# Kernel optimization log

Hardware: AMD Instinct MI355X
Metric: run time of the kernel (lower is better)

## Reference

```python
import jax, jax.numpy as jnp
import numpy as np

B, C, H, W = 16, 1, 128, 8192
N_MAX = 128
CHIRP_W, PERIOD = 48, 64
W_OUT = N_MAX * CHIRP_W + (N_MAX - 1)  # 6271 compacted columns (chirps + separators)
SEP_CLASS_ID = 2


def setup_inputs() -> dict:
    key = jax.random.key(0)
    k1, k2, k3, k4 = jax.random.split(key, 4)
    x = jax.random.normal(k1, (B, C, H, W), dtype=jnp.float32)
    starts = jnp.arange(N_MAX, dtype=jnp.int32) * PERIOD
    xi = jnp.stack([starts, starts + CHIRP_W], axis=-1)           # (N_MAX, 2)
    xi = jnp.broadcast_to(xi[None], (B, N_MAX, 2)).astype(jnp.int32)
    N = jax.random.randint(k2, (B,), 96, N_MAX + 1, dtype=jnp.int32)
    N = N.at[0].set(N_MAX)  # pin so static W_OUT equals torch's dynamic int(w_max.max())
    xl = jax.random.randint(k3, (B, W), 0, 2, dtype=jnp.int32)
    sep_param = jax.random.normal(k4, (1, 1, 1), dtype=jnp.float32)
    return {"x": x, "xi": xi, "N": N, "xl": xl, "sep_param": sep_param, "w_out": W_OUT}


def _compactify(x, xi, N, xl, sep_param, w_out):
    """Vectorized TinyBird.compactify_data: remove silence, keep chirp blocks,
    insert one separator column between consecutive valid chirps."""
    Bx, Cx, Hx, Wx = x.shape
    n_max = xi.shape[1]
    idx = jnp.arange(n_max, dtype=jnp.int32)[None, :]             # (1, N_max)
    Nb = N.reshape(-1, 1).astype(jnp.int32)
    valid = idx < Nb                                              # (B, N_max)

    s0, e0 = xi[..., 0], xi[..., 1]
    w = jnp.clip(e0 - s0, 0, None)
    w_valid = jnp.where(valid, w, 0)
    csum = jnp.cumsum(w_valid, axis=1)
    sn = csum - w_valid + idx                                     # new start (seps before = idx)
    en = csum + idx                                               # new end
    xi_new = jnp.where(valid[..., None], jnp.stack([sn, en], -1), 0).astype(xi.dtype)

    BIG = jnp.int32(1 << 30)
    en_srt = jnp.where(valid, en, BIG)                            # strictly increasing over valid part
    t = jnp.arange(w_out, dtype=jnp.int32)[None, :]               # (1, w_out)
    # i = number of chirp ends <= t  ->  chirp whose [sn_i, en_i) may contain t
    i = (en_srt[:, :, None] <= t[:, None, :]).sum(axis=1).astype(jnp.int32)  # (B, w_out)
    ic = jnp.clip(i, 0, n_max - 1)
    take = lambda a: jnp.take_along_axis(a, ic, axis=1)
    sn_i, en_i = take(sn), take(en)
    s0_i, e0_i = take(s0), take(e0)
    in_chirp = (i < Nb) & (t >= sn_i) & (en_i > sn_i) & (e0_i > s0_i)
    src = jnp.clip(s0_i + (t - sn_i), 0, Wx - 1)                  # (B, w_out)

    # separator column: t == en_{i-1}, previous chirp is not the last valid one, en < W
    jp = jnp.clip(i - 1, 0, n_max - 1)
    en_prev = jnp.take_along_axis(en, jp, axis=1)
    is_sep = (i >= 1) & (t == en_prev) & ((i - 1) < (Nb - 1)) & (en_prev < Wx)

    x_g = jnp.take_along_axis(x, src[:, None, None, :], axis=3)   # (B, C, H, w_out)
    sep = sep_param[0, 0, 0]
    x_new = jnp.where(in_chirp[:, None, None, :], x_g,
                      jnp.where(is_sep[:, None, None, :], sep, jnp.float32(0)))
    xl_g = jnp.take_along_axis(xl, src, axis=1)
    xl_new = jnp.where(in_chirp, xl_g,
                       jnp.where(is_sep, jnp.asarray(SEP_CLASS_ID, xl.dtype),
                                 jnp.asarray(0, xl.dtype)))
    return x_new, xi_new, xl_new


def reference(x, xi, N, xl, sep_param, w_out):
    return _compactify(x, xi, N, xl, sep_param, w_out)
```

## Files before the change

kernel.cpp:

```cpp
#include <hip/hip_runtime.h>

#define BB     16
#define HH     128
#define WW     8192
#define N_MAXC 128
#define W_OUTC 6271
#define SEP_CLASS 2.0f

#define X_ELEMS (BB * HH * W_OUTC)
#define XI_OFF  (X_ELEMS)
#define XL_OFF  (X_ELEMS + BB * N_MAXC * 2)

#define MAP_BYTES ((size_t)(BB * W_OUTC) * sizeof(int))

#define TCOLS  1024
#define HROWS  16
#define MTILE  896

__global__ __launch_bounds__(256) void tb_meta(const int* __restrict__ xi,
                                               const int* __restrict__ Nv,
                                               const int* __restrict__ xl,
                                               float* __restrict__ out,
                                               int* __restrict__ map) {
    __shared__ int s_s0[N_MAXC], s_e0[N_MAXC], s_scan[N_MAXC], s_sn[N_MAXC], s_en[N_MAXC];
    const int b   = blockIdx.x;
    const int tid = threadIdx.x;
    const int Nb  = Nv[b];

    int wv = 0;
    if (tid < N_MAXC) {
        int2 se = ((const int2*)xi)[b * N_MAXC + tid];
        s_s0[tid] = se.x; s_e0[tid] = se.y;
        int w = se.y - se.x; if (w < 0) w = 0;
        wv = (tid < Nb) ? w : 0;
        s_scan[tid] = wv;
    }
    __syncthreads();
    #pragma unroll
    for (int off = 1; off < N_MAXC; off <<= 1) {
        int v = 0;
        if (tid < N_MAXC && tid >= off) v = s_scan[tid - off];
        __syncthreads();
        if (tid < N_MAXC) s_scan[tid] += v;
        __syncthreads();
    }
    if (tid < N_MAXC) {
        int c = s_scan[tid];
        s_sn[tid] = c - wv + tid;
        s_en[tid] = c + tid;
    }
    __syncthreads();

    if (blockIdx.y == 0 && tid < N_MAXC) {
        const bool valid = tid < Nb;
        out[XI_OFF + (b * N_MAXC + tid) * 2 + 0] = valid ? (float)s_sn[tid] : 0.0f;
        out[XI_OFF + (b * N_MAXC + tid) * 2 + 1] = valid ? (float)s_en[tid] : 0.0f;
    }

    const int t_lo = blockIdx.y * MTILE;
    const int t_hi = (t_lo + MTILE < W_OUTC) ? t_lo + MTILE : W_OUTC;
    for (int t = t_lo + tid; t < t_hi; t += 256) {
        int lo = 0, hi = Nb;
        while (lo < hi) { int mid = (lo + hi) >> 1; if (s_en[mid] <= t) lo = mid + 1; else hi = mid; }
        const int i  = lo;
        const int ic = (i < N_MAXC - 1) ? i : (N_MAXC - 1);
        int m = -2;
        if (i < Nb) {
            int sn = s_sn[ic], en = s_en[ic];
            if (t >= sn && en > sn && s_e0[ic] > s_s0[ic]) {
                int src = s_s0[ic] + (t - sn);
                src = src < 0 ? 0 : (src > WW - 1 ? WW - 1 : src);
                m = src;
            }
        }
        if (m == -2 && i >= 1) {
            int ep = s_en[i - 1];
            if (t == ep && (i - 1) < (Nb - 1) && ep < WW) m = -1;
        }
        if (map) map[b * W_OUTC + t] = m;
        float v = (m >= 0) ? (float)xl[b * WW + m] : ((m == -1) ? SEP_CLASS : 0.0f);
        out[XL_OFF + b * W_OUTC + t] = v;
    }
}

__global__ __launch_bounds__(256) void tb_gather(const float* __restrict__ x,
                                                 const int* __restrict__ map,
                                                 const float* __restrict__ sep_param,
                                                 float* __restrict__ out) {
    __shared__ int s_map[TCOLS];
    const int t0   = blockIdx.x * TCOLS;
    const int h0   = blockIdx.y * HROWS;
    const int b    = blockIdx.z;
    const int tid  = threadIdx.x;
    const int tmax = W_OUTC - t0;
    const float sep = sep_param[0];

    for (int j = tid; j < TCOLS; j += 256) {
        int t = t0 + j;
        s_map[j] = (t < W_OUTC) ? map[b * W_OUTC + t] : -2;
    }
    __syncthreads();

    const float* xb = x   + (size_t)(b * HH + h0) * WW;
    float*       ob = out + (size_t)(b * HH + h0) * W_OUTC + t0;

    if (tmax >= TCOLS) {
        #pragma unroll 4
        for (int r = 0; r < HROWS; ++r) {
            const float* xr   = xb + (size_t)r * WW;
            float*       orow = ob + (size_t)r * W_OUTC;
            #pragma unroll
            for (int k = 0; k < 4; ++k) {
                const int j = k * 256 + tid;
                const int m = s_map[j];
                const int a = (m >= 0) ? m : 0;
                const float xv = xr[a];
                orow[j] = (m >= 0) ? xv : ((m == -1) ? sep : 0.0f);
            }
        }
    } else {
        #pragma unroll 4
        for (int r = 0; r < HROWS; ++r) {
            const float* xr   = xb + (size_t)r * WW;
            float*       orow = ob + (size_t)r * W_OUTC;
            #pragma unroll
            for (int k = 0; k < 4; ++k) {
                const int j = k * 256 + tid;
                if (j < tmax) {
                    const int m = s_map[j];
                    const int a = (m >= 0) ? m : 0;
                    const float xv = xr[a];
                    orow[j] = (m >= 0) ? xv : ((m == -1) ? sep : 0.0f);
                }
            }
        }
    }
}

#define FTILE   512
#define FHCHUNK 32

__device__ __forceinline__ void fb_scan(const int* __restrict__ xi, int b, int Nb,
                                        int* s_s0, int* s_e0, int* s_sn, int* s_en, int tid) {
    if (tid < N_MAXC) {
        s_s0[tid] = xi[(b * N_MAXC + tid) * 2 + 0];
        s_e0[tid] = xi[(b * N_MAXC + tid) * 2 + 1];
    }
    __syncthreads();
    if (tid == 0) {
        int c = 0;
        for (int i = 0; i < N_MAXC; ++i) {
            int w = s_e0[i] - s_s0[i]; if (w < 0) w = 0;
            int wvv = (i < Nb) ? w : 0;
            c += wvv;
            s_sn[i] = c - wvv + i;
            s_en[i] = c + i;
        }
    }
    __syncthreads();
}

__global__ __launch_bounds__(256) void tb_gather_tiled(const float* __restrict__ x,
                                                       const int* __restrict__ xi,
                                                       const int* __restrict__ Nv,
                                                       const float* __restrict__ sep_param,
                                                       float* __restrict__ out) {
    __shared__ int s_s0[N_MAXC], s_e0[N_MAXC], s_sn[N_MAXC], s_en[N_MAXC];
    __shared__ int s_map[FTILE];
    const int b = blockIdx.z, h0 = blockIdx.y * FHCHUNK, t0 = blockIdx.x * FTILE;
    const int tid = threadIdx.x, Nb = Nv[b];
    fb_scan(xi, b, Nb, s_s0, s_e0, s_sn, s_en, tid);
    for (int j = tid; j < FTILE; j += 256) {
        int t = t0 + j, m = -2;
        if (t < W_OUTC) {
            int lo = 0, hi = Nb;
            while (lo < hi) { int mid = (lo + hi) >> 1; if (s_en[mid] <= t) lo = mid + 1; else hi = mid; }
            int i = lo, ic = (i < N_MAXC - 1) ? i : (N_MAXC - 1);
            if (i < Nb) {
                int sn = s_sn[ic], en = s_en[ic];
                if (t >= sn && en > sn && s_e0[ic] > s_s0[ic]) {
                    int src = s_s0[ic] + (t - sn);
                    m = src < 0 ? 0 : (src > WW - 1 ? WW - 1 : src);
                }
            }
            if (m == -2 && i >= 1) {
                int ep = s_en[i - 1];
                if (t == ep && (i - 1) < (Nb - 1) && ep < WW) m = -1;
            }
        }
        s_map[j] = m;
    }
    __syncthreads();
    const float sep = sep_param[0];
    const float* xb = x + (size_t)b * HH * WW;
    float* ob = out + (size_t)b * HH * W_OUTC;
    for (int r = 0; r < FHCHUNK; ++r) {
        const int h = h0 + r;
        const float* xr = xb + (size_t)h * WW;
        float* orow = ob + (size_t)h * W_OUTC;
        for (int j = tid; j < FTILE; j += 256) {
            int t = t0 + j;
            if (t < W_OUTC) {
                int m = s_map[j];
                orow[t] = (m >= 0) ? xr[m] : ((m == -1) ? sep : 0.0f);
            }
        }
    }
}

extern "C" void kernel_launch(void* const* d_in, const int* in_sizes, int n_in,
                              void* d_out, int out_size, void* d_ws, size_t ws_size,
                              hipStream_t stream) {
    const float* x   = (const float*)d_in[0];
    const int*   xi  = (const int*)  d_in[1];
    const int*   Nv  = (const int*)  d_in[2];
    const int*   xl  = (const int*)  d_in[3];
    const float* sep = (const float*)d_in[4];
    float*       out = (float*)d_out;

    const bool use_ws = (ws_size >= MAP_BYTES) && (d_ws != nullptr);
    int* map = use_ws ? (int*)d_ws : nullptr;

    tb_meta<<<dim3(BB, 7), dim3(256), 0, stream>>>(xi, Nv, xl, out, map);

    if (use_ws) {
        dim3 grid((W_OUTC + TCOLS - 1) / TCOLS, HH / HROWS, BB);
        tb_gather<<<grid, dim3(256), 0, stream>>>(x, map, sep, out);
    } else {
        dim3 grid((W_OUTC + FTILE - 1) / FTILE, HH / FHCHUNK, BB);
        tb_gather_tiled<<<grid, dim3(256), 0, stream>>>(x, xi, Nv, sep, out);
    }
}
```

Before: 153.0 us.

## Flatten gather into float4 output stores with batched loads per thread

Replaces the 2D-tiled gather that staged the column map in shared memory with a flat grid-stride kernel. Each thread handles eight 4-element output chunks, loading all map entries and gathered x values up front before issuing float4 stores, which raises memory-level parallelism and widens the writes. The meta kernel's tile is shrunk so it launches more blocks. In exchange, map reads now go to global memory (cached) rather than shared, per-element index math includes integer division, and the row-wrap handling is needed because W_OUT is odd, so a float4 chunk can span two rows.

```diff
diff --git a/kernel.cpp b/kernel.cpp
--- a/kernel.cpp
+++ b/kernel.cpp
@@ -10,12 +10,15 @@
 #define X_ELEMS (BB * HH * W_OUTC)
 #define XI_OFF  (X_ELEMS)
 #define XL_OFF  (X_ELEMS + BB * N_MAXC * 2)
+#define NCHUNKS (X_ELEMS / 4)
 
 #define MAP_BYTES ((size_t)(BB * W_OUTC) * sizeof(int))
 
-#define TCOLS  1024
-#define HROWS  16
-#define MTILE  896
+#define GBLK  1568
+#define GSTR  (GBLK * 256)
+#define GITER 8
+
+#define MTILE 512
 
 __global__ __launch_bounds__(256) void tb_meta(const int* __restrict__ xi,
                                                const int* __restrict__ Nv,
@@ -83,82 +86,64 @@
     }
 }
 
-__global__ __launch_bounds__(256) void tb_gather(const float* __restrict__ x,
-                                                 const int* __restrict__ map,
-                                                 const float* __restrict__ sep_param,
-                                                 float* __restrict__ out) {
-    __shared__ int s_map[TCOLS];
-    const int t0   = blockIdx.x * TCOLS;
-    const int h0   = blockIdx.y * HROWS;
-    const int b    = blockIdx.z;
-    const int tid  = threadIdx.x;
-    const int tmax = W_OUTC - t0;
+__global__ __launch_bounds__(256) void tb_gather_flat(const float* __restrict__ x,
+                                                      const int* __restrict__ map,
+                                                      const float* __restrict__ sep_param,
+                                                      float* __restrict__ out) {
+    const unsigned gtid = blockIdx.x * 256u + threadIdx.x;
     const float sep = sep_param[0];
 
-    for (int j = tid; j < TCOLS; j += 256) {
-        int t = t0 + j;
-        s_map[j] = (t < W_OUTC) ? map[b * W_OUTC + t] : -2;
-    }
-    __syncthreads();
-
-    const float* xb = x   + (size_t)(b * HH + h0) * WW;
-    float*       ob = out + (size_t)(b * HH + h0) * W_OUTC + t0;
-
-    if (tmax >= TCOLS) {
-        #pragma unroll 4
-        for (int r = 0; r < HROWS; ++r) {
-            const float* xr   = xb + (size_t)r * WW;
-            float*       orow = ob + (size_t)r * W_OUTC;
-            #pragma unroll
-            for (int k = 0; k < 4; ++k) {
-                const int j = k * 256 + tid;
-                const int m = s_map[j];
-                const int a = (m >= 0) ? m : 0;
-                const float xv = xr[a];
-                orow[j] = (m >= 0) ? xv : ((m == -1) ? sep : 0.0f);
-            }
-        }
-    } else {
-        #pragma unroll 4
-        for (int r = 0; r < HROWS; ++r) {
-            const float* xr   = xb + (size_t)r * WW;
-            float*       orow = ob + (size_t)r * W_OUTC;
-            #pragma unroll
-            for (int k = 0; k < 4; ++k) {
-                const int j = k * 256 + tid;
-                if (j < tmax) {
-                    const int m = s_map[j];
-                    const int a = (m >= 0) ? m : 0;
-                    const float xv = xr[a];
-                    orow[j] = (m >= 0) ? xv : ((m == -1) ? sep : 0.0f);
-                }
-            }
+    unsigned rowA[GITER], colA[GITER];
+    int      mv[GITER][4];
+    float    xv[GITER][4];
+
+    #pragma unroll
+    for (int j = 0; j < GITER; ++j) {
+        unsigned c = gtid + (unsigned)j * (unsigned)GSTR;
+        if (c >= (unsigned)NCHUNKS) c = NCHUNKS - 1;
+        const unsigned flat = c * 4u;
+        const unsigned bh   = flat / (unsigned)W_OUTC;
+        rowA[j] = bh;
+        colA[j] = flat - bh * (unsigned)W_OUTC;
+    }
+    #pragma unroll
+    for (int j = 0; j < GITER; ++j) {
+        #pragma unroll
+        for (int k = 0; k < 4; ++k) {
+            unsigned tk = colA[j] + (unsigned)k;
+            unsigned r  = rowA[j];
+            if (tk >= (unsigned)W_OUTC) { tk -= (unsigned)W_OUTC; r += 1u; }
+            mv[j][k] = map[(r >> 7) * (unsigned)W_OUTC + tk];
+        }
+    }
+    #pragma unroll
+    for (int j = 0; j < GITER; ++j) {
+        #pragma unroll
+        for (int k = 0; k < 4; ++k) {
+            unsigned tk = colA[j] + (unsigned)k;
+            unsigned r  = rowA[j];
+            if (tk >= (unsigned)W_OUTC) r += 1u;
+            const int m = mv[j][k];
+            const unsigned a = (m >= 0) ? (unsigned)m : 0u;
+            xv[j][k] = x[((size_t)r << 13) + a];
+        }
+    }
+    #pragma unroll
+    for (int j = 0; j < GITER; ++j) {
+        const unsigned c = gtid + (unsigned)j * (unsigned)GSTR;
+        if (c < (unsigned)NCHUNKS) {
+            float4 v;
+            v.x = (mv[j][0] >= 0) ? xv[j][0] : ((mv[j][0] == -1) ? sep : 0.0f);
+            v.y = (mv[j][1] >= 0) ? xv[j][1] : ((mv[j][1] == -1) ? sep : 0.0f);
+            v.z = (mv[j][2] >= 0) ? xv[j][2] : ((mv[j][2] == -1) ? sep : 0.0f);
+            v.w = (mv[j][3] >= 0) ? xv[j][3] : ((mv[j][3] == -1) ? sep : 0.0f);
+            ((float4*)out)[c] = v;
         }
     }
 }
 
 #define FTILE   512
 #define FHCHUNK 32
-
-__device__ __forceinline__ void fb_scan(const int* __restrict__ xi, int b, int Nb,
-                                        int* s_s0, int* s_e0, int* s_sn, int* s_en, int tid) {
-    if (tid < N_MAXC) {
-        s_s0[tid] = xi[(b * N_MAXC + tid) * 2 + 0];
-        s_e0[tid] = xi[(b * N_MAXC + tid) * 2 + 1];
-    }
-    __syncthreads();
-    if (tid == 0) {
-        int c = 0;
-        for (int i = 0; i < N_MAXC; ++i) {
-            int w = s_e0[i] - s_s0[i]; if (w < 0) w = 0;
-            int wvv = (i < Nb) ? w : 0;
-            c += wvv;
-            s_sn[i] = c - wvv + i;
-            s_en[i] = c + i;
-        }
-    }
-    __syncthreads();
-}
 
 __global__ __launch_bounds__(256) void tb_gather_tiled(const float* __restrict__ x,
                                                        const int* __restrict__ xi,
@@ -169,7 +154,22 @@
     __shared__ int s_map[FTILE];
     const int b = blockIdx.z, h0 = blockIdx.y * FHCHUNK, t0 = blockIdx.x * FTILE;
     const int tid = threadIdx.x, Nb = Nv[b];
-    fb_scan(xi, b, Nb, s_s0, s_e0, s_sn, s_en, tid);
+    if (tid < N_MAXC) {
+        s_s0[tid] = xi[(b * N_MAXC + tid) * 2 + 0];
+        s_e0[tid] = xi[(b * N_MAXC + tid) * 2 + 1];
+    }
+    __syncthreads();
+    if (tid == 0) {
+        int c = 0;
+        for (int i = 0; i < N_MAXC; ++i) {
+            int w = s_e0[i] - s_s0[i]; if (w < 0) w = 0;
+            int wvv = (i < Nb) ? w : 0;
+            c += wvv;
+            s_sn[i] = c - wvv + i;
+            s_en[i] = c + i;
+        }
+    }
+    __syncthreads();
     for (int j = tid; j < FTILE; j += 256) {
         int t = t0 + j, m = -2;
         if (t < W_OUTC) {
@@ -221,11 +221,10 @@
     const bool use_ws = (ws_size >= MAP_BYTES) && (d_ws != nullptr);
     int* map = use_ws ? (int*)d_ws : nullptr;
 
-    tb_meta<<<dim3(BB, 7), dim3(256), 0, stream>>>(xi, Nv, xl, out, map);
+    tb_meta<<<dim3(BB, 13), dim3(256), 0, stream>>>(xi, Nv, xl, out, map);
 
     if (use_ws) {
-        dim3 grid((W_OUTC + TCOLS - 1) / TCOLS, HH / HROWS, BB);
-        tb_gather<<<grid, dim3(256), 0, stream>>>(x, map, sep, out);
+        tb_gather_flat<<<dim3(GBLK), dim3(256), 0, stream>>>(x, map, sep, out);
     } else {
         dim3 grid((W_OUTC + FTILE - 1) / FTILE, HH / FHCHUNK, BB);
         tb_gather_tiled<<<grid, dim3(256), 0, stream>>>(x, xi, Nv, sep, out);
```

Result: faster. 135.6 us (-11.4%).
